# Kernel optimization log

Hardware: AMD Instinct MI355X
Metric: run time of the kernel (lower is better)

The kernel has to match this reference:

```python
import jax, jax.numpy as jnp
import numpy as np
from jax import lax

Q = 0.707  # torchaudio default Q for lowpass/highpass_biquad

def _shift(x, k):
    # delay along time axis by k samples, zero-padded (zero initial conditions)
    pad = jnp.zeros(x.shape[:-1] + (k,), x.dtype)
    return jnp.concatenate([pad, x[..., :-k]], axis=-1)

def _iir2(ff, a1, a2):
    # y[n] = ff[n] - a1*y[n-1] - a2*y[n-2], zero init state; scan over time
    ff_t = jnp.moveaxis(ff, -1, 0)              # [T, B, C]
    y0 = jnp.zeros(ff.shape[:-1], ff.dtype)     # [B, C]
    def step(carry, f):
        y1, y2 = carry
        y = f - a1 * y1 - a2 * y2
        return (y, y1), y
    _, y = lax.scan(step, (y0, y0), ff_t)
    return jnp.moveaxis(y, 0, -1)

def _biquad(x, b0, b1, b2, a0, a1, a2):
    # torchaudio.functional.biquad: normalize all coeffs by a0, then lfilter
    b0, b1, b2 = b0 / a0, b1 / a0, b2 / a0
    a1, a2 = a1 / a0, a2 / a0
    ff = b0 * x + b1 * _shift(x, 1) + b2 * _shift(x, 2)  # FIR part, vectorized
    return _iir2(ff, a1, a2)

def _lowpass_biquad(x, sr, cutoff):
    w0 = 2.0 * jnp.pi * cutoff / sr
    cos_w0 = jnp.cos(w0)
    alpha = jnp.sin(w0) / (2.0 * Q)
    b0 = (1.0 - cos_w0) / 2.0
    b1 = 1.0 - cos_w0
    b2 = b0
    a0 = 1.0 + alpha
    a1 = -2.0 * cos_w0
    a2 = 1.0 - alpha
    return _biquad(x, b0, b1, b2, a0, a1, a2)

def _highpass_biquad(x, sr, cutoff):
    w0 = 2.0 * jnp.pi * cutoff / sr
    cos_w0 = jnp.cos(w0)
    alpha = jnp.sin(w0) / (2.0 * Q)
    b0 = (1.0 + cos_w0) / 2.0
    b1 = -(1.0 + cos_w0)
    b2 = b0
    a0 = 1.0 + alpha
    a1 = -2.0 * cos_w0
    a2 = 1.0 - alpha
    return _biquad(x, b0, b1, b2, a0, a1, a2)

def setup_inputs() -> dict:
    key = jax.random.key(0)
    k1, = jax.random.split(key, 1)
    audio = jax.random.normal(k1, (32, 2, 220500), dtype=jnp.float32) * 0.1
    return {
        "audio": audio,
        "sample_rate": 44100,
        "cutoff_low": jnp.float32(200.0),
        "cutoff_high": jnp.float32(5000.0),
    }

def reference(audio, sample_rate, cutoff_low, cutoff_high):
    sr = jnp.float32(sample_rate)
    audio_low = _lowpass_biquad(audio, sr, cutoff_low)
    audio_high = _highpass_biquad(audio, sr, cutoff_high)
    return audio_low - audio_high
```

## Files before the change

### kernel.cpp

```cpp
#include <hip/hip_runtime.h>
#include <math.h>

#define T_LEN  220500
#define SEG    64
#define TPB    256
#define WPB    4
#define WARML  8
#define WOUT   ((64 - WARML) * SEG)
#define BOUT   (WPB * WOUT)
#define PRE    (WARML * SEG + 4)
#define RSAMP  (BOUT + PRE)
#define SLOT(j) ((j) + ((((j) >> 6)) << 2))
#define LDSW   (SLOT(RSAMP - 1) + 1)

__global__ __launch_bounds__(TPB, 2) void bandpass_kernel(
    const float* __restrict__ x,
    const int* __restrict__ sr_p,
    const float* __restrict__ fl_p,
    const float* __restrict__ fh_p,
    float* __restrict__ out)
{
    __shared__ float lds[LDSW];

    const int tid  = threadIdx.x;
    const int lane = tid & 63;
    const int wv   = tid >> 6;
    const int seq  = blockIdx.y;
    const int bxi  = blockIdx.x;

    const float sr   = (float)sr_p[0];
    const float twoQ = (float)(2.0 * 0.707);

    float w0 = (float)(2.0 * M_PI) * fl_p[0] / sr;
    float cw = cosf(w0);
    float al = sinf(w0) / twoQ;
    float a0 = 1.0f + al;
    const float lb0  = (1.0f - cw) * 0.5f / a0;
    const float lb1  = (1.0f - cw) / a0;
    const float lb2  = lb0;
    const float lna1 = 2.0f * cw / a0;
    const float lna2 = -(1.0f - al) / a0;

    w0 = (float)(2.0 * M_PI) * fh_p[0] / sr;
    cw = cosf(w0);
    al = sinf(w0) / twoQ;
    a0 = 1.0f + al;
    const float hb0  = (1.0f + cw) * 0.5f / a0;
    const float hb1  = -(1.0f + cw) / a0;
    const float hb2  = hb0;
    const float hna1 = 2.0f * cw / a0;
    const float hna2 = -(1.0f - al) / a0;

    float4 Ml[4], Mh[4];
    {
        float a = lna1, b = lna2, c = 1.0f, d = 0.0f;
#pragma unroll
        for (int i = 0; i < 6; ++i) {
            float t0 = fmaf(a, a, b * c), t1 = fmaf(a, b, b * d);
            float t2 = fmaf(c, a, d * c), t3 = fmaf(c, b, d * d);
            a = t0; b = t1; c = t2; d = t3;
        }
        Ml[0] = make_float4(a, b, c, d);
#pragma unroll
        for (int k = 1; k < 4; ++k) {
            float t0 = fmaf(a, a, b * c), t1 = fmaf(a, b, b * d);
            float t2 = fmaf(c, a, d * c), t3 = fmaf(c, b, d * d);
            a = t0; b = t1; c = t2; d = t3;
            Ml[k] = make_float4(a, b, c, d);
        }
        a = hna1; b = hna2; c = 1.0f; d = 0.0f;
#pragma unroll
        for (int i = 0; i < 6; ++i) {
            float t0 = fmaf(a, a, b * c), t1 = fmaf(a, b, b * d);
            float t2 = fmaf(c, a, d * c), t3 = fmaf(c, b, d * d);
            a = t0; b = t1; c = t2; d = t3;
        }
        Mh[0] = make_float4(a, b, c, d);
#pragma unroll
        for (int k = 1; k < 4; ++k) {
            float t0 = fmaf(a, a, b * c), t1 = fmaf(a, b, b * d);
            float t2 = fmaf(c, a, d * c), t3 = fmaf(c, b, d * d);
            a = t0; b = t1; c = t2; d = t3;
            Mh[k] = make_float4(a, b, c, d);
        }
    }

    const float* __restrict__ xs = x   + (size_t)seq * T_LEN;
    float*       __restrict__ os = out + (size_t)seq * T_LEN;

    const int G0 = bxi * BOUT - PRE;

    for (int j4 = tid; j4 < RSAMP / 4; j4 += TPB) {
        const int j = j4 * 4;
        const int g = G0 + j;
        float4 v;
        if (g >= 0 && g + 4 <= T_LEN) {
            v = *(const float4*)(xs + g);
        } else {
            float e[4];
#pragma unroll
            for (int k = 0; k < 4; ++k) {
                const int gg = g + k;
                e[k] = (gg >= 0 && gg < T_LEN) ? xs[gg] : 0.f;
            }
            v = make_float4(e[0], e[1], e[2], e[3]);
        }
        *(float4*)&lds[SLOT(j)] = v;
    }
    __syncthreads();

    const int jb = 4 + wv * WOUT + lane * SEG;

    const float xh1 = lds[SLOT(jb - 1)];
    const float xh2 = lds[SLOT(jb - 2)];

    float x1 = xh1, x2 = xh2;
    float ly1 = 0.f, ly2 = 0.f, hy1 = 0.f, hy2 = 0.f;
#pragma unroll
    for (int i = 0; i < 16; ++i) {
        const float4 xv = *(const float4*)&lds[SLOT(jb + 4 * i)];
        const float xa[4] = {xv.x, xv.y, xv.z, xv.w};
#pragma unroll
        for (int k = 0; k < 4; ++k) {
            const float xc  = xa[k];
            const float ffl = fmaf(lb0, xc, fmaf(lb1, x1, lb2 * x2));
            const float yl  = fmaf(lna2, ly2, fmaf(lna1, ly1, ffl));
            const float ffh = fmaf(hb0, xc, fmaf(hb1, x1, hb2 * x2));
            const float yh  = fmaf(hna2, hy2, fmaf(hna1, hy1, ffh));
            ly2 = ly1; ly1 = yl; hy2 = hy1; hy1 = yh;
            x2 = x1; x1 = xc;
        }
    }

    float4 p = make_float4(ly1, ly2, hy1, hy2);
#pragma unroll
    for (int k = 0; k < 4; ++k) {
        const int d = 1 << k;
        float qx = __shfl_up(p.x, d, 64);
        float qy = __shfl_up(p.y, d, 64);
        float qz = __shfl_up(p.z, d, 64);
        float qw = __shfl_up(p.w, d, 64);
        if (lane < d) { qx = 0.f; qy = 0.f; qz = 0.f; qw = 0.f; }
        p.x = fmaf(Ml[k].x, qx, fmaf(Ml[k].y, qy, p.x));
        p.y = fmaf(Ml[k].z, qx, fmaf(Ml[k].w, qy, p.y));
        p.z = fmaf(Mh[k].x, qz, fmaf(Mh[k].y, qw, p.z));
        p.w = fmaf(Mh[k].z, qz, fmaf(Mh[k].w, qw, p.w));
    }
    float sx0 = __shfl_up(p.x, 1, 64);
    float sx1 = __shfl_up(p.y, 1, 64);
    float sx2 = __shfl_up(p.z, 1, 64);
    float sx3 = __shfl_up(p.w, 1, 64);
    if (lane == 0) { sx0 = 0.f; sx1 = 0.f; sx2 = 0.f; sx3 = 0.f; }

    __syncthreads();

    if (lane >= WARML) {
        float bx1 = xh1, bx2 = xh2;
        float Ly1 = sx0, Ly2 = sx1, Hy1 = sx2, Hy2 = sx3;
#pragma unroll
        for (int i = 0; i < 16; ++i) {
            float* sp = &lds[SLOT(jb + 4 * i)];
            const float4 xv = *(const float4*)sp;
            const float xa[4] = {xv.x, xv.y, xv.z, xv.w};
            float o[4];
#pragma unroll
            for (int k = 0; k < 4; ++k) {
                const float xc  = xa[k];
                const float ffl = fmaf(lb0, xc, fmaf(lb1, bx1, lb2 * bx2));
                const float yl  = fmaf(lna2, Ly2, fmaf(lna1, Ly1, ffl));
                const float ffh = fmaf(hb0, xc, fmaf(hb1, bx1, hb2 * bx2));
                const float yh  = fmaf(hna2, Hy2, fmaf(hna1, Hy1, ffh));
                Ly2 = Ly1; Ly1 = yl; Hy2 = Hy1; Hy1 = yh;
                bx2 = bx1; bx1 = xc;
                o[k] = yl - yh;
            }
            *(float4*)sp = make_float4(o[0], o[1], o[2], o[3]);
        }
    }
    __syncthreads();

    for (int f4 = tid; f4 < BOUT / 4; f4 += TPB) {
        const int j = PRE + 4 * f4;
        const int g = G0 + j;
        if (g < T_LEN) {
            *(float4*)(os + g) = *(const float4*)&lds[SLOT(j)];
        }
    }
}

extern "C" void kernel_launch(void* const* d_in, const int* in_sizes, int n_in,
                              void* d_out, int out_size, void* d_ws, size_t ws_size,
                              hipStream_t stream) {
    const float* x  = (const float*)d_in[0];
    const int*   sr = (const int*)d_in[1];
    const float* fl = (const float*)d_in[2];
    const float* fh = (const float*)d_in[3];
    float* outp = (float*)d_out;

    const int nseq = in_sizes[0] / T_LEN;
    const int bxn  = (T_LEN + BOUT - 1) / BOUT;

    dim3 block(TPB);
    dim3 grid(bxn, nseq);
    hipLaunchKernelGGL(bandpass_kernel, grid, block, 0, stream,
                       x, sr, fl, fh, outp);
}
```

Baseline: 128.9 us.

## Use single-wave blocks loading inputs directly to registers instead of LDS staging

Shrinks each block to one 64-lane wave handling one window and loads each lane's 64-sample segment straight from global memory into registers, fetching the halo samples by lane shuffle. LDS is now used only to transpose outputs into coalesced stores, with an XOR swizzle to avoid bank conflicts. The per-step transition matrices are computed on the fly inside the scan instead of being precomputed. This removes the LDS input round trip and several block-wide barriers, but per-lane strided global loads are uncoalesced and 64 floats of input per lane raise register pressure.

```diff
diff --git a/kernel.cpp b/kernel.cpp
--- a/kernel.cpp
+++ b/kernel.cpp
@@ -3,30 +3,26 @@
 
 #define T_LEN  220500
 #define SEG    64
-#define TPB    256
-#define WPB    4
+#define TPB    64
 #define WARML  8
 #define WOUT   ((64 - WARML) * SEG)
-#define BOUT   (WPB * WOUT)
-#define PRE    (WARML * SEG + 4)
-#define RSAMP  (BOUT + PRE)
-#define SLOT(j) ((j) + ((((j) >> 6)) << 2))
-#define LDSW   (SLOT(RSAMP - 1) + 1)
+#define WSLOTS (WOUT / 4)
+#define NWIN   ((T_LEN + WOUT - 1) / WOUT)
 
-__global__ __launch_bounds__(TPB, 2) void bandpass_kernel(
+__device__ __forceinline__ int swz(int s) { return s ^ ((s >> 4) & 7); }
+
+__global__ __launch_bounds__(TPB) void bandpass_kernel(
     const float* __restrict__ x,
     const int* __restrict__ sr_p,
     const float* __restrict__ fl_p,
     const float* __restrict__ fh_p,
     float* __restrict__ out)
 {
-    __shared__ float lds[LDSW];
+    __shared__ float4 lds4[WSLOTS];
 
-    const int tid  = threadIdx.x;
-    const int lane = tid & 63;
-    const int wv   = tid >> 6;
+    const int lane = threadIdx.x;
+    const int win  = blockIdx.x;
     const int seq  = blockIdx.y;
-    const int bxi  = blockIdx.x;
 
     const float sr   = (float)sr_p[0];
     const float twoQ = (float)(2.0 * 0.707);
@@ -51,75 +47,34 @@
     const float hna1 = 2.0f * cw / a0;
     const float hna2 = -(1.0f - al) / a0;
 
-    float4 Ml[4], Mh[4];
-    {
-        float a = lna1, b = lna2, c = 1.0f, d = 0.0f;
-#pragma unroll
-        for (int i = 0; i < 6; ++i) {
-            float t0 = fmaf(a, a, b * c), t1 = fmaf(a, b, b * d);
-            float t2 = fmaf(c, a, d * c), t3 = fmaf(c, b, d * d);
-            a = t0; b = t1; c = t2; d = t3;
-        }
-        Ml[0] = make_float4(a, b, c, d);
-#pragma unroll
-        for (int k = 1; k < 4; ++k) {
-            float t0 = fmaf(a, a, b * c), t1 = fmaf(a, b, b * d);
-            float t2 = fmaf(c, a, d * c), t3 = fmaf(c, b, d * d);
-            a = t0; b = t1; c = t2; d = t3;
-            Ml[k] = make_float4(a, b, c, d);
-        }
-        a = hna1; b = hna2; c = 1.0f; d = 0.0f;
-#pragma unroll
-        for (int i = 0; i < 6; ++i) {
-            float t0 = fmaf(a, a, b * c), t1 = fmaf(a, b, b * d);
-            float t2 = fmaf(c, a, d * c), t3 = fmaf(c, b, d * d);
-            a = t0; b = t1; c = t2; d = t3;
-        }
-        Mh[0] = make_float4(a, b, c, d);
-#pragma unroll
-        for (int k = 1; k < 4; ++k) {
-            float t0 = fmaf(a, a, b * c), t1 = fmaf(a, b, b * d);
-            float t2 = fmaf(c, a, d * c), t3 = fmaf(c, b, d * d);
-            a = t0; b = t1; c = t2; d = t3;
-            Mh[k] = make_float4(a, b, c, d);
-        }
-    }
-
     const float* __restrict__ xs = x   + (size_t)seq * T_LEN;
     float*       __restrict__ os = out + (size_t)seq * T_LEN;
 
-    const int G0 = bxi * BOUT - PRE;
+    const int Wbase = win * WOUT;
+    const int s0    = Wbase - WARML * SEG + lane * SEG;
 
-    for (int j4 = tid; j4 < RSAMP / 4; j4 += TPB) {
-        const int j = j4 * 4;
-        const int g = G0 + j;
-        float4 v;
-        if (g >= 0 && g + 4 <= T_LEN) {
-            v = *(const float4*)(xs + g);
-        } else {
-            float e[4];
+    float4 xr[16];
 #pragma unroll
-            for (int k = 0; k < 4; ++k) {
-                const int gg = g + k;
-                e[k] = (gg >= 0 && gg < T_LEN) ? xs[gg] : 0.f;
-            }
-            v = make_float4(e[0], e[1], e[2], e[3]);
-        }
-        *(float4*)&lds[SLOT(j)] = v;
+    for (int i = 0; i < 16; ++i) {
+        const int g  = s0 + 4 * i;
+        const int gc = min(max(g, 0), T_LEN - 4);
+        float4 v = *(const float4*)(xs + gc);
+        if (g < 0 || g >= T_LEN) v = make_float4(0.f, 0.f, 0.f, 0.f);
+        xr[i] = v;
     }
-    __syncthreads();
 
-    const int jb = 4 + wv * WOUT + lane * SEG;
-
-    const float xh1 = lds[SLOT(jb - 1)];
-    const float xh2 = lds[SLOT(jb - 2)];
+    float xh1 = __shfl_up(xr[15].w, 1, 64);
+    float xh2 = __shfl_up(xr[15].z, 1, 64);
+    if (lane == 0) {
+        xh1 = (s0 >= 1) ? xs[s0 - 1] : 0.f;
+        xh2 = (s0 >= 2) ? xs[s0 - 2] : 0.f;
+    }
 
     float x1 = xh1, x2 = xh2;
     float ly1 = 0.f, ly2 = 0.f, hy1 = 0.f, hy2 = 0.f;
 #pragma unroll
     for (int i = 0; i < 16; ++i) {
-        const float4 xv = *(const float4*)&lds[SLOT(jb + 4 * i)];
-        const float xa[4] = {xv.x, xv.y, xv.z, xv.w};
+        const float xa[4] = {xr[i].x, xr[i].y, xr[i].z, xr[i].w};
 #pragma unroll
         for (int k = 0; k < 4; ++k) {
             const float xc  = xa[k];
@@ -132,6 +87,18 @@
         }
     }
 
+    float la = lna1, lb = lna2, lc = 1.0f, ld = 0.0f;
+    float ha = hna1, hb = hna2, hc = 1.0f, hd = 0.0f;
+#pragma unroll
+    for (int i = 0; i < 6; ++i) {
+        float t0 = fmaf(la, la, lb * lc), t1 = fmaf(la, lb, lb * ld);
+        float t2 = fmaf(lc, la, ld * lc), t3 = fmaf(lc, lb, ld * ld);
+        la = t0; lb = t1; lc = t2; ld = t3;
+        t0 = fmaf(ha, ha, hb * hc); t1 = fmaf(ha, hb, hb * hd);
+        t2 = fmaf(hc, ha, hd * hc); t3 = fmaf(hc, hb, hd * hd);
+        ha = t0; hb = t1; hc = t2; hd = t3;
+    }
+
     float4 p = make_float4(ly1, ly2, hy1, hy2);
 #pragma unroll
     for (int k = 0; k < 4; ++k) {
@@ -141,10 +108,16 @@
         float qz = __shfl_up(p.z, d, 64);
         float qw = __shfl_up(p.w, d, 64);
         if (lane < d) { qx = 0.f; qy = 0.f; qz = 0.f; qw = 0.f; }
-        p.x = fmaf(Ml[k].x, qx, fmaf(Ml[k].y, qy, p.x));
-        p.y = fmaf(Ml[k].z, qx, fmaf(Ml[k].w, qy, p.y));
-        p.z = fmaf(Mh[k].x, qz, fmaf(Mh[k].y, qw, p.z));
-        p.w = fmaf(Mh[k].z, qz, fmaf(Mh[k].w, qw, p.w));
+        p.x = fmaf(la, qx, fmaf(lb, qy, p.x));
+        p.y = fmaf(lc, qx, fmaf(ld, qy, p.y));
+        p.z = fmaf(ha, qz, fmaf(hb, qw, p.z));
+        p.w = fmaf(hc, qz, fmaf(hd, qw, p.w));
+        float t0 = fmaf(la, la, lb * lc), t1 = fmaf(la, lb, lb * ld);
+        float t2 = fmaf(lc, la, ld * lc), t3 = fmaf(lc, lb, ld * ld);
+        la = t0; lb = t1; lc = t2; ld = t3;
+        t0 = fmaf(ha, ha, hb * hc); t1 = fmaf(ha, hb, hb * hd);
+        t2 = fmaf(hc, ha, hd * hc); t3 = fmaf(hc, hb, hd * hd);
+        ha = t0; hb = t1; hc = t2; hd = t3;
     }
     float sx0 = __shfl_up(p.x, 1, 64);
     float sx1 = __shfl_up(p.y, 1, 64);
@@ -152,16 +125,13 @@
     float sx3 = __shfl_up(p.w, 1, 64);
     if (lane == 0) { sx0 = 0.f; sx1 = 0.f; sx2 = 0.f; sx3 = 0.f; }
 
-    __syncthreads();
-
     if (lane >= WARML) {
         float bx1 = xh1, bx2 = xh2;
         float Ly1 = sx0, Ly2 = sx1, Hy1 = sx2, Hy2 = sx3;
+        const int sb = (lane - WARML) * 16;
 #pragma unroll
         for (int i = 0; i < 16; ++i) {
-            float* sp = &lds[SLOT(jb + 4 * i)];
-            const float4 xv = *(const float4*)sp;
-            const float xa[4] = {xv.x, xv.y, xv.z, xv.w};
+            const float xa[4] = {xr[i].x, xr[i].y, xr[i].z, xr[i].w};
             float o[4];
 #pragma unroll
             for (int k = 0; k < 4; ++k) {
@@ -174,17 +144,18 @@
                 bx2 = bx1; bx1 = xc;
                 o[k] = yl - yh;
             }
-            *(float4*)sp = make_float4(o[0], o[1], o[2], o[3]);
+            lds4[swz(sb + i)] = make_float4(o[0], o[1], o[2], o[3]);
         }
     }
+
     __syncthreads();
 
-    for (int f4 = tid; f4 < BOUT / 4; f4 += TPB) {
-        const int j = PRE + 4 * f4;
-        const int g = G0 + j;
-        if (g < T_LEN) {
-            *(float4*)(os + g) = *(const float4*)&lds[SLOT(j)];
-        }
+#pragma unroll
+    for (int k = 0; k < WSLOTS / 64; ++k) {
+        const int slot = 64 * k + lane;
+        const float4 v = lds4[swz(slot)];
+        const int g = Wbase + 4 * slot;
+        if (g < T_LEN) *(float4*)(os + g) = v;
     }
 }
 
@@ -198,10 +169,9 @@
     float* outp = (float*)d_out;
 
     const int nseq = in_sizes[0] / T_LEN;
-    const int bxn  = (T_LEN + BOUT - 1) / BOUT;
 
     dim3 block(TPB);
-    dim3 grid(bxn, nseq);
+    dim3 grid(NWIN, nseq);
     hipLaunchKernelGGL(bandpass_kernel, grid, block, 0, stream,
                        x, sr, fl, fh, outp);
 }
```

New measurement: 118.4 us. -8.1%, faster.
